# Kernel tuning notes

Hardware: AMD Instinct MI355X
Metric: run time of the kernel (lower is better)

## Reference

```python
import jax, jax.numpy as jnp
import numpy as np
import math

B, T = 2, 1024
D_MODEL = 1024
N_HEAD = 16
HEAD_DIM = D_MODEL // N_HEAD
VOCAB = 32000
NUM_LOOP = 4
EPS_LN = 1e-5                       # torch LayerNorm default
EPS_RMS = float(np.finfo(np.float32).eps)  # torch RMSNorm eps=None -> finfo eps


def setup_inputs() -> dict:
    key = jax.random.key(0)
    ks = jax.random.split(key, 12)
    s = 0.02
    d = D_MODEL
    tok = jax.random.normal(ks[1], (VOCAB, d), jnp.float32) * s
    tok = tok.at[0].set(0.0)  # padding_idx=0
    return {
        "idx": jax.random.randint(ks[0], (B, T), 0, VOCAB),
        "tok_embed": tok,
        "ln_e_g": jnp.ones((d,), jnp.float32),
        "ln_e_b": jnp.zeros((d,), jnp.float32),
        "Wqkv": jax.random.normal(ks[2], (d, 3 * d), jnp.float32) * s,
        "bqkv": jnp.zeros((3 * d,), jnp.float32),
        "Wo": jax.random.normal(ks[3], (d, d), jnp.float32) * s,
        "bo": jnp.zeros((d,), jnp.float32),
        "W1": jax.random.normal(ks[4], (d, 4 * d), jnp.float32) * s,
        "b1": jnp.zeros((4 * d,), jnp.float32),
        "W2": jax.random.normal(ks[5], (4 * d, d), jnp.float32) * s,
        "b2": jnp.zeros((d,), jnp.float32),
        "n1_w": jnp.ones((d,), jnp.float32),
        "n2_w": jnp.ones((d,), jnp.float32),
        "lnf_g": jnp.ones((d,), jnp.float32),
        "lnf_b": jnp.zeros((d,), jnp.float32),
        "Wlm": jax.random.normal(ks[6], (d, VOCAB), jnp.float32) * s,
        "blm": jnp.zeros((VOCAB,), jnp.float32),
    }


def layernorm(x, g, b):
    m = jnp.mean(x, axis=-1, keepdims=True)
    v = jnp.mean(jnp.square(x - m), axis=-1, keepdims=True)
    return (x - m) * jax.lax.rsqrt(v + EPS_LN) * g + b


def rmsnorm(x, w):
    ms = jnp.mean(jnp.square(x), axis=-1, keepdims=True)
    return x * jax.lax.rsqrt(ms + EPS_RMS) * w


def gelu_tanh(x):
    c = math.sqrt(2.0 / math.pi)
    return 0.5 * x * (1.0 + jnp.tanh(c * (x + 0.044715 * x * x * x)))


def alibi_causal_bias(t):
    # rpe[q,k] = -(q-k) for q>k else 0, scaled per head by 2^(-8/H*(h+1)); causal -inf above diag
    pos = jnp.arange(t)
    rel = pos[:, None] - pos[None, :]                      # [T,T] = q - k
    slopes = 2.0 ** (-8.0 / N_HEAD * jnp.arange(1, N_HEAD + 1, dtype=jnp.float32))
    bias = -slopes[:, None, None] * rel.astype(jnp.float32)  # [H,T,T]
    return jnp.where(rel[None] >= 0, bias, -jnp.inf)       # causal mask fused


def reference(idx, tok_embed, ln_e_g, ln_e_b, Wqkv, bqkv, Wo, bo,
              W1, b1, W2, b2, n1_w, n2_w, lnf_g, lnf_b, Wlm, blm):
    b, t = idx.shape
    x = layernorm(tok_embed[idx], ln_e_g, ln_e_b)          # rpe=True: no sinusoidal PE
    bias = alibi_causal_bias(t)                            # [H,T,T]
    scale = 1.0 / math.sqrt(HEAD_DIM)

    for _ in range(NUM_LOOP):
        # attention sublayer
        h = rmsnorm(x, n1_w)
        qkv = h @ Wqkv + bqkv
        q, k, v = jnp.split(qkv, 3, axis=-1)
        q = q.reshape(b, t, N_HEAD, HEAD_DIM).transpose(0, 2, 1, 3)
        k = k.reshape(b, t, N_HEAD, HEAD_DIM).transpose(0, 2, 1, 3)
        v = v.reshape(b, t, N_HEAD, HEAD_DIM).transpose(0, 2, 1, 3)
        att = jnp.einsum('bhqd,bhkd->bhqk', q, k) * scale + bias[None]
        att = jax.nn.softmax(att, axis=-1)
        y = jnp.einsum('bhqk,bhkd->bhqd', att, v)
        y = y.transpose(0, 2, 1, 3).reshape(b, t, D_MODEL)
        x = x + (y @ Wo + bo)
        # mlp sublayer
        h = rmsnorm(x, n2_w)
        x = x + (gelu_tanh(h @ W1 + b1) @ W2 + b2)

    x = layernorm(x, lnf_g, lnf_b)
    return x @ Wlm + blm  # [B,T,VOCAB]
```

## Files before the change

### kernel.cpp

```cpp
#include <hip/hip_runtime.h>
#include <stdint.h>

#define DEVI __device__ __forceinline__

typedef __attribute__((ext_vector_type(8))) short short8;
typedef __attribute__((ext_vector_type(4))) float f32x4;
typedef unsigned short u16;
typedef unsigned int u32;

typedef const __attribute__((address_space(1))) void* gas_ptr;
typedef __attribute__((address_space(3))) void* las_ptr;

constexpr int BBATCH = 2;
constexpr int TT  = 1024;
constexpr int BT  = BBATCH * TT;
constexpr int DM  = 1024;
constexpr int NH  = 16;
constexpr int HD  = 64;
constexpr int DFF = 4096;
constexpr int NV  = 32000;
constexpr int NL  = 4;

DEVI u16 f2b(float f) {
  u32 u = __builtin_bit_cast(u32, f);
  u = (u + 0x7fffu + ((u >> 16) & 1u)) >> 16;
  return (u16)u;
}
DEVI float b2f(u16 h) { return __builtin_bit_cast(float, (u32)h << 16); }

DEVI void gld16(const void* g, void* l) {
  __builtin_amdgcn_global_load_lds((gas_ptr)g, (las_ptr)l, 16, 0, 0);
}

DEVI float wave_sum(float v) {
#pragma unroll
  for (int off = 32; off; off >>= 1) v += __shfl_xor(v, off);
  return v;
}
DEVI float block_sum(float v, float* sb) {
  v = wave_sum(v);
  int lane = threadIdx.x & 63, wid = threadIdx.x >> 6;
  __syncthreads();
  if (lane == 0) sb[wid] = v;
  __syncthreads();
  return sb[0] + sb[1] + sb[2] + sb[3];
}

DEVI float gelu_f(float x) {
  float u = 0.7978845608028654f * (x + 0.044715f * x * x * x);
  float e = __expf(2.0f * u);
  return x * (1.0f - 1.0f / (e + 1.0f));
}

__global__ __launch_bounds__(256) void wt_transpose_all(
    const float* __restrict__ Wqkv, const float* __restrict__ Wo,
    const float* __restrict__ W1, const float* __restrict__ W2,
    const float* __restrict__ Wlm,
    u16* __restrict__ WqkvT, u16* __restrict__ WoT, u16* __restrict__ W1T,
    u16* __restrict__ W2T, u16* __restrict__ WlmT) {
  __shared__ float t[32][33];
  int bid = blockIdx.x;
  const float* in; u16* out; int K, N, tt;
  if (bid < 3072)       { in = Wqkv; out = WqkvT; K = 1024; N = 3072;  tt = bid; }
  else if (bid < 4096)  { in = Wo;   out = WoT;   K = 1024; N = 1024;  tt = bid - 3072; }
  else if (bid < 8192)  { in = W1;   out = W1T;   K = 1024; N = 4096;  tt = bid - 4096; }
  else if (bid < 12288) { in = W2;   out = W2T;   K = 4096; N = 1024;  tt = bid - 8192; }
  else                  { in = Wlm;  out = WlmT;  K = 1024; N = 32000; tt = bid - 12288; }
  int nx = N >> 5;
  int n0 = (tt % nx) * 32, k0 = (tt / nx) * 32;
  int tx = threadIdx.x & 31, ty = threadIdx.x >> 5;
#pragma unroll
  for (int i = 0; i < 4; ++i)
    t[ty + 8 * i][tx] = in[(size_t)(k0 + ty + 8 * i) * N + n0 + tx];
  __syncthreads();
#pragma unroll
  for (int i = 0; i < 4; ++i)
    out[(size_t)(n0 + ty + 8 * i) * K + k0 + tx] = f2b(t[tx][ty + 8 * i]);
}

__global__ __launch_bounds__(256) void embed_ln_k(const int* __restrict__ idx,
                                                  const float* __restrict__ tok,
                                                  const float* __restrict__ g,
                                                  const float* __restrict__ b,
                                                  float* __restrict__ x) {
  __shared__ float sb[4];
  int row = blockIdx.x, tid = threadIdx.x;
  float4 v = ((const float4*)(tok + (size_t)idx[row] * DM))[tid];
  float s = block_sum(v.x + v.y + v.z + v.w, sb);
  float m = s * (1.0f / DM);
  float dx = v.x - m, dy = v.y - m, dz = v.z - m, dw = v.w - m;
  float q = block_sum(dx * dx + dy * dy + dz * dz + dw * dw, sb);
  float rs = rsqrtf(q * (1.0f / DM) + 1e-5f);
  float4 gg = ((const float4*)g)[tid];
  float4 bb = ((const float4*)b)[tid];
  float4 o = make_float4(dx * rs * gg.x + bb.x, dy * rs * gg.y + bb.y,
                         dz * rs * gg.z + bb.z, dw * rs * gg.w + bb.w);
  ((float4*)(x + (size_t)row * DM))[tid] = o;
}

__global__ __launch_bounds__(256) void final_ln_k(const float* __restrict__ x,
                                                  const float* __restrict__ g,
                                                  const float* __restrict__ b,
                                                  u16* __restrict__ xf) {
  __shared__ float sb[4];
  int row = blockIdx.x, tid = threadIdx.x;
  float4 v = ((const float4*)(x + (size_t)row * DM))[tid];
  float s = block_sum(v.x + v.y + v.z + v.w, sb);
  float m = s * (1.0f / DM);
  float dx = v.x - m, dy = v.y - m, dz = v.z - m, dw = v.w - m;
  float q = block_sum(dx * dx + dy * dy + dz * dz + dw * dw, sb);
  float rs = rsqrtf(q * (1.0f / DM) + 1e-5f);
  float4 gg = ((const float4*)g)[tid];
  float4 bb = ((const float4*)b)[tid];
  u32 lo = (u32)f2b(dx * rs * gg.x + bb.x) | ((u32)f2b(dy * rs * gg.y + bb.y) << 16);
  u32 hi = (u32)f2b(dz * rs * gg.z + bb.z) | ((u32)f2b(dw * rs * gg.w + bb.w) << 16);
  ((uint2*)(xf + (size_t)row * DM))[tid] = make_uint2(lo, hi);
}

__global__ __launch_bounds__(256) void rmsnorm_k(const float* __restrict__ x,
                                                 const float* __restrict__ w,
                                                 u16* __restrict__ h) {
  __shared__ float sb[4];
  int row = blockIdx.x, tid = threadIdx.x;
  float4 v = ((const float4*)(x + (size_t)row * DM))[tid];
  float q = block_sum(v.x * v.x + v.y * v.y + v.z * v.z + v.w * v.w, sb);
  float rs = rsqrtf(q * (1.0f / DM) + 1.1920928955078125e-7f);
  float4 ww = ((const float4*)w)[tid];
  u32 lo = (u32)f2b(v.x * rs * ww.x) | ((u32)f2b(v.y * rs * ww.y) << 16);
  u32 hi = (u32)f2b(v.z * rs * ww.z) | ((u32)f2b(v.w * rs * ww.w) << 16);
  ((uint2*)(h + (size_t)row * DM))[tid] = make_uint2(lo, hi);
}

__global__ __launch_bounds__(256) void attn_k(const u16* __restrict__ qkv,
                                              const u16* __restrict__ vT,
                                              u16* __restrict__ y) {
  __shared__ __align__(16) char sP[16384];
  __shared__ __align__(16) char sK[16384];
  __shared__ __align__(16) char sV[16384];
  const int tid = threadIdx.x, lane = tid & 63, wid = tid >> 6;
  const int bid = blockIdx.x;
  const int sl = (bid + (bid >> 8)) & 15;
  const int qt = (sl & 1) ? (sl >> 1) : (15 - (sl >> 1));
  const int bh = (bid >> 4) & 31, b = bh >> 4, h = bh & 15;
  const int nt = (qt >> 1) + 1;
  const float slope = exp2f(-0.5f * (float)(h + 1));

  const char* Qb = (const char*)(qkv + (size_t)b * TT * 3 * DM + h * HD);
  const char* Kb = (const char*)(qkv + (size_t)b * TT * 3 * DM + DM + h * HD);
  const char* Vb = (const char*)(vT + (size_t)bh * HD * TT);

#pragma unroll
  for (int ci = 0; ci < 2; ++ci) {
    int c = wid * 2 + ci;
    int r = c * 8 + (lane >> 3);
    int q = (lane & 7) ^ (r & 7);
    gld16(Qb + (size_t)(qt * 64 + r) * 6144 + q * 16, sP + c * 1024 + lane * 16);
  }

  auto stageKV = [&](int kt) {
    int kv0 = kt * 128;
#pragma unroll
    for (int ci = 0; ci < 4; ++ci) {
      int c = wid * 4 + ci;
      int r = c * 8 + (lane >> 3);
      int q = (lane & 7) ^ (r & 7);
      gld16(Kb + (size_t)(kv0 + r) * 6144 + q * 16, sK + c * 1024 + lane * 16);
    }
#pragma unroll
    for (int ci = 0; ci < 4; ++ci) {
      int c = wid * 4 + ci;
      int d = c * 4 + (lane >> 4);
      int q = (lane & 15) ^ (d & 15);
      gld16(Vb + (size_t)d * 2048 + (size_t)kv0 * 2 + q * 16, sV + c * 1024 + lane * 16);
    }
  };
  stageKV(0);
  asm volatile("s_waitcnt vmcnt(8)" ::: "memory");

  short8 qf[2];
#pragma unroll
  for (int ks = 0; ks < 2; ++ks) {
    int r = wid * 16 + (lane & 15);
    int q = ((ks << 2) + (lane >> 4)) ^ (r & 7);
    qf[ks] = *(const short8*)(sP + r * 128 + q * 16);
  }

  f32x4 Y[4] = {};
  float m_r[4], l_r[4];
#pragma unroll
  for (int r = 0; r < 4; ++r) { m_r[r] = -3e38f; l_r[r] = 0.0f; }

  for (int kt = 0; kt < nt; ++kt) {
    asm volatile("s_waitcnt vmcnt(0)" ::: "memory");
    __syncthreads();

    f32x4 s[8] = {};
    __builtin_amdgcn_s_setprio(1);
#pragma unroll
    for (int ks = 0; ks < 2; ++ks) {
      short8 kf[8];
#pragma unroll
      for (int j = 0; j < 8; ++j) {
        int r = j * 16 + (lane & 15);
        int q = ((ks << 2) + (lane >> 4)) ^ (r & 7);
        kf[j] = *(const short8*)(sK + r * 128 + q * 16);
      }
#pragma unroll
      for (int j = 0; j < 8; ++j)
        s[j] = __builtin_amdgcn_mfma_f32_16x16x32_bf16(qf[ks], kf[j], s[j], 0, 0, 0);
    }
    __builtin_amdgcn_s_setprio(0);

    const int kv0 = kt * 128;
    const int qbase = qt * 64 + wid * 16 + ((lane >> 4) << 2);
    float rowmax[4] = {-3e38f, -3e38f, -3e38f, -3e38f};
#pragma unroll
    for (int j = 0; j < 8; ++j) {
      int kcol = kv0 + j * 16 + (lane & 15);
#pragma unroll
      for (int r = 0; r < 4; ++r) {
        int qrow = qbase + r;
        float v = (kcol <= qrow) ? s[j][r] * 0.125f - slope * (float)(qrow - kcol) : -3e38f;
        s[j][r] = v;
        rowmax[r] = fmaxf(rowmax[r], v);
      }
    }
#pragma unroll
    for (int r = 0; r < 4; ++r) {
      rowmax[r] = fmaxf(rowmax[r], __shfl_xor(rowmax[r], 1));
      rowmax[r] = fmaxf(rowmax[r], __shfl_xor(rowmax[r], 2));
      rowmax[r] = fmaxf(rowmax[r], __shfl_xor(rowmax[r], 4));
      rowmax[r] = fmaxf(rowmax[r], __shfl_xor(rowmax[r], 8));
      float mn = fmaxf(m_r[r], rowmax[r]);
      float al = __expf(m_r[r] - mn);
      m_r[r] = mn;
      l_r[r] *= al;
#pragma unroll
      for (int j = 0; j < 4; ++j) Y[j][r] *= al;
    }
    float rs[4] = {0.0f, 0.0f, 0.0f, 0.0f};
#pragma unroll
    for (int j = 0; j < 8; ++j)
#pragma unroll
      for (int r = 0; r < 4; ++r) {
        float p = __expf(s[j][r] - m_r[r]);
        s[j][r] = p;
        rs[r] += p;
      }
#pragma unroll
    for (int r = 0; r < 4; ++r) {
      rs[r] += __shfl_xor(rs[r], 1);
      rs[r] += __shfl_xor(rs[r], 2);
      rs[r] += __shfl_xor(rs[r], 4);
      rs[r] += __shfl_xor(rs[r], 8);
      l_r[r] += rs[r];
    }
#pragma unroll
    for (int j = 0; j < 8; ++j)
#pragma unroll
      for (int r = 0; r < 4; ++r) {
        int rl = wid * 16 + ((lane >> 4) << 2) + r;
        int c = j * 16 + (lane & 15);
        int g = c >> 3;
        *(u16*)(sP + rl * 256 + ((g ^ (rl & 15)) << 4) + (c & 7) * 2) = f2b(s[j][r]);
      }

    __builtin_amdgcn_s_setprio(1);
#pragma unroll
    for (int ks = 0; ks < 4; ++ks) {
      short8 pf, vf[4];
      {
        int r = wid * 16 + (lane & 15);
        int q = ((ks << 2) + (lane >> 4)) ^ (r & 15);
        pf = *(const short8*)(sP + r * 256 + (q << 4));
      }
#pragma unroll
      for (int j = 0; j < 4; ++j) {
        int d = j * 16 + (lane & 15);
        int q = ((ks << 2) + (lane >> 4)) ^ (d & 15);
        vf[j] = *(const short8*)(sV + d * 256 + (q << 4));
      }
#pragma unroll
      for (int j = 0; j < 4; ++j)
        Y[j] = __builtin_amdgcn_mfma_f32_16x16x32_bf16(pf, vf[j], Y[j], 0, 0, 0);
    }
    __builtin_amdgcn_s_setprio(0);
    __syncthreads();
    if (kt + 1 < nt) stageKV(kt + 1);
  }

#pragma unroll
  for (int r = 0; r < 4; ++r) {
    float inv = 1.0f / l_r[r];
    int qrow = qt * 64 + wid * 16 + ((lane >> 4) << 2) + r;
    u16* yp = y + (size_t)(b * TT + qrow) * DM + h * HD;
#pragma unroll
    for (int j = 0; j < 4; ++j)
      yp[j * 16 + (lane & 15)] = f2b(Y[j][r] * inv);
  }
}

enum { EPI_BF16 = 0, EPI_GELU = 1, EPI_ADDF32 = 2, EPI_F32 = 3, EPI_ATOMIC = 4, EPI_QKV = 5 };

template <int BM, int BN, int WM, int WN, int EPI, int KS = 1>
__global__ __launch_bounds__(256, 2) void gemm_bt(
    const u16* __restrict__ A, int lda, const u16* __restrict__ Bt, int ldb,
    const float* __restrict__ bias, void* __restrict__ C, int ldc,
    float* __restrict__ resid, int K, u16* __restrict__ vTout) {
  constexpr int BK = 64;
  constexpr int NW = WM * WN;
  constexpr int FM = BM / WM / 16, FN = BN / WN / 16;
  constexpr int ABYTES = BM * BK * 2, BBYTES = BN * BK * 2;
  constexpr int ACH = ABYTES / 1024, BCH = BBYTES / 1024, NCH = ACH + BCH;
  extern __shared__ __align__(16) char smem[];

  const int tid = threadIdx.x, lane = tid & 63, wid = tid >> 6;
  const int brow = blockIdx.y * BM, bcol = blockIdx.x * BN;
  const long long kbase2 = (long long)blockIdx.z * (K / KS) * 2;

  const int nt = (K / KS) >> 6;
  const int widm = wid / WN, widn = wid % WN;
  const int rm0 = widm * (BM / WM), cn0 = widn * (BN / WN);

  f32x4 acc[FM][FN] = {};

  const int swq16 = (((lane & 7) ^ ((lane >> 3) & 7)) << 4);
  const int lrow8 = lane >> 3;

  auto stage = [&](int buf, int kt) {
    char* base = smem + buf * (ABYTES + BBYTES);
    const char* Ag = (const char*)A;
    const char* Bg = (const char*)Bt;
    long long kOff = kbase2 + (long long)kt * 128 + swq16;
#pragma unroll
    for (int ci = 0; ci < NCH / NW; ++ci) {
      int c = wid + ci * NW;
      if (c < ACH) {
        int r = c * 8 + lrow8;
        gld16(Ag + (long long)(brow + r) * (lda * 2) + kOff, base + c * 1024 + lane * 16);
      } else {
        int r = (c - ACH) * 8 + lrow8;
        gld16(Bg + (long long)(bcol + r) * (ldb * 2) + kOff,
              base + ABYTES + (c - ACH) * 1024 + lane * 16);
      }
    }
  };

  auto compute = [&](int buf) {
    char* baseA = smem + buf * (ABYTES + BBYTES);
    char* baseB = baseA + ABYTES;
#pragma unroll
    for (int ks = 0; ks < 2; ++ks) {
      short8 af[FM], bv[FN];
#pragma unroll
      for (int i = 0; i < FM; ++i) {
        int r = rm0 + i * 16 + (lane & 15);
        int cq = ((ks << 2) + (lane >> 4)) ^ (r & 7);
        af[i] = *(const short8*)(baseA + r * 128 + (cq << 4));
      }
#pragma unroll
      for (int j = 0; j < FN; ++j) {
        int r = cn0 + j * 16 + (lane & 15);
        int cq = ((ks << 2) + (lane >> 4)) ^ (r & 7);
        bv[j] = *(const short8*)(baseB + r * 128 + (cq << 4));
      }
#pragma unroll
      for (int i = 0; i < FM; ++i)
#pragma unroll
        for (int j = 0; j < FN; ++j)
          acc[i][j] = __builtin_amdgcn_mfma_f32_16x16x32_bf16(af[i], bv[j], acc[i][j], 0, 0, 0);
    }
  };

  stage(0, 0);
  __syncthreads();
  int cur = 0;
  for (int t = 0; t < nt; ++t) {
    if (t + 1 < nt) stage(cur ^ 1, t + 1);
    compute(cur);
    __syncthreads();
    cur ^= 1;
  }

  if constexpr (EPI == EPI_QKV) {
    if (bcol >= 2 * DM) {
      u16* st = (u16*)smem;
#pragma unroll
      for (int i = 0; i < FM; ++i)
#pragma unroll
        for (int j = 0; j < FN; ++j)
#pragma unroll
          for (int r = 0; r < 4; ++r) {
            int rl = rm0 + i * 16 + ((lane >> 4) << 2) + r;
            int cl = cn0 + j * 16 + (lane & 15);
            st[rl * 130 + cl] = f2b(acc[i][j][r] + bias[bcol + cl]);
          }
      __syncthreads();
      const int b = brow >> 10, t0b = brow & (TT - 1);
      const int h0 = (bcol - 2 * DM) >> 6;
      const int sub = tid & 15;
#pragma unroll
      for (int pass = 0; pass < 8; ++pass) {
        int d = pass * 16 + (tid >> 4);
        u32 pk[4];
#pragma unroll
        for (int k2 = 0; k2 < 4; ++k2) {
          u16 lo = st[(sub * 8 + 2 * k2) * 130 + d];
          u16 hi = st[(sub * 8 + 2 * k2 + 1) * 130 + d];
          pk[k2] = (u32)lo | ((u32)hi << 16);
        }
        int head = h0 + (d >> 6), dd = d & 63;
        *(uint4*)(vTout + ((size_t)((b * NH + head) * HD + dd)) * TT + t0b + sub * 8) =
            make_uint4(pk[0], pk[1], pk[2], pk[3]);
      }
      return;
    }
  }

  const int r0 = brow + rm0 + ((lane >> 4) << 2);
  const int c0 = bcol + cn0 + (lane & 15);
#pragma unroll
  for (int i = 0; i < FM; ++i) {
#pragma unroll
    for (int j = 0; j < FN; ++j) {
#pragma unroll
      for (int r = 0; r < 4; ++r) {
        int row = r0 + i * 16 + r;
        int col = c0 + j * 16;
        float v = acc[i][j][r];
        if constexpr (EPI == EPI_BF16 || EPI == EPI_QKV) {
          ((u16*)C)[(size_t)row * ldc + col] = f2b(v + bias[col]);
        } else if constexpr (EPI == EPI_GELU) {
          ((u16*)C)[(size_t)row * ldc + col] = f2b(gelu_f(v + bias[col]));
        } else if constexpr (EPI == EPI_ADDF32) {
          size_t o = (size_t)row * ldc + col;
          resid[o] += v + bias[col];
        } else if constexpr (EPI == EPI_ATOMIC) {
          size_t o = (size_t)row * ldc + col;
          atomicAdd(&resid[o], v + (blockIdx.z == 0 ? bias[col] : 0.0f));
        } else {
          ((float*)C)[(size_t)row * ldc + col] = v + bias[col];
        }
      }
    }
  }
}

template <int EPI>
__global__ __launch_bounds__(512, 2) void gemm8(
    const u16* __restrict__ A, int lda, const u16* __restrict__ Bt, int ldb,
    const float* __restrict__ bias, void* __restrict__ C, int ldc, int K, int nby) {
  __shared__ __align__(16) char smem[2][2][32768];
  const int tid = threadIdx.x, lane = tid & 63;
  const int wid = tid >> 6, wm = wid >> 2, wn = wid & 3;

  const int nb = gridDim.x;
  const int q8 = nb >> 3, r8 = nb & 7;
  const int xcd = blockIdx.x & 7, lin = blockIdx.x >> 3;
  const int idx = (xcd < r8 ? xcd * (q8 + 1) : r8 * (q8 + 1) + (xcd - r8) * q8) + lin;
  const int brow = (idx % nby) * 256, bcol = (idx / nby) * 256;

  const int nt = K >> 6, niter = nt >> 1;

  const int srow = tid >> 3, sq = tid & 7;
  auto stage = [&](int buf, int isB, int half, int kt) {
    const u16* G = isB ? Bt : A;
    const int ld = isB ? ldb : lda;
    const int base = isB ? bcol : brow;
    char* L = &smem[buf][isB][half * 16384];
#pragma unroll
    for (int l = 0; l < 2; ++l) {
      int rl = half * 128 + l * 64 + srow;
      gld16((const char*)G + (size_t)(base + rl) * (ld * 2) + kt * 128 + ((sq ^ (rl & 7)) << 4),
            L + l * 8192 + tid * 16);
    }
  };

  short8 bfr[4][2], afr[2][2];
  f32x4 acc[8][4] = {};

  stage(0, 0, 0, 0); stage(0, 0, 1, 0);
  stage(0, 1, 0, 0); stage(0, 1, 1, 0);
  stage(1, 1, 0, 1); stage(1, 1, 1, 1);
  asm volatile("s_waitcnt vmcnt(0)" ::: "memory");
  __builtin_amdgcn_s_barrier();

  for (int i = 0; i < niter; ++i) {
    const bool full = (i + 1 < niter);
    const int t2 = 2 * i + 2, t3 = 2 * i + 3;
#pragma unroll
    for (int h = 0; h < 2; ++h) {
#pragma unroll
      for (int qd = 0; qd < 4; ++qd) {
        if (qd == 0) {
#pragma unroll
          for (int j = 0; j < 4; ++j)
#pragma unroll
            for (int ks = 0; ks < 2; ++ks) {
              int r = wn * 64 + j * 16 + (lane & 15);
              int q = ((ks << 2) + (lane >> 4)) ^ (r & 7);
              bfr[j][ks] = *(const short8*)&smem[h][1][r * 128 + q * 16];
            }
        }
#pragma unroll
        for (int f = 0; f < 2; ++f)
#pragma unroll
          for (int ks = 0; ks < 2; ++ks) {
            int r = wm * 128 + (qd * 2 + f) * 16 + (lane & 15);
            int q = ((ks << 2) + (lane >> 4)) ^ (r & 7);
            afr[f][ks] = *(const short8*)&smem[h][0][r * 128 + q * 16];
          }
        if (h == 0) {
          if (qd == 0) stage(1, 0, 0, 2 * i + 1);
          else if (qd == 1) stage(1, 0, 1, 2 * i + 1);
          else if (qd == 2) { if (full) stage(0, 1, 0, t2); }
          else              { if (full) stage(0, 1, 1, t2); }
        } else {
          if (qd == 0)      { if (full) stage(0, 0, 0, t2); }
          else if (qd == 1) { if (full) stage(0, 0, 1, t2); }
          else if (qd == 2) { if (full) stage(1, 1, 0, t3); }
          else              { if (full) stage(1, 1, 1, t3); }
        }
        if (qd == 3) {
          if (full) asm volatile("s_waitcnt vmcnt(4)" ::: "memory");
          else if (h == 0) asm volatile("s_waitcnt vmcnt(0)" ::: "memory");
        }
        __builtin_amdgcn_s_barrier();
        asm volatile("s_waitcnt lgkmcnt(0)" ::: "memory");
        __builtin_amdgcn_s_setprio(1);
#pragma unroll
        for (int f = 0; f < 2; ++f)
#pragma unroll
          for (int j = 0; j < 4; ++j)
#pragma unroll
            for (int ks = 0; ks < 2; ++ks)
              acc[qd * 2 + f][j] = __builtin_amdgcn_mfma_f32_16x16x32_bf16(
                  afr[f][ks], bfr[j][ks], acc[qd * 2 + f][j], 0, 0, 0);
        __builtin_amdgcn_s_setprio(0);
        __builtin_amdgcn_s_barrier();
      }
    }
  }

  if constexpr (EPI == EPI_F32) {
    char* sf = &smem[0][0][0];
    float* C32 = (float*)C;
#pragma unroll
    for (int half = 0; half < 2; ++half) {
      if (wm == half) {
#pragma unroll
        for (int fi = 0; fi < 8; ++fi)
#pragma unroll
          for (int j = 0; j < 4; ++j) {
            int cl = wn * 64 + j * 16 + (lane & 15);
            float bv = bias[bcol + cl];
            int qsw = (cl >> 2);
#pragma unroll
            for (int r = 0; r < 4; ++r) {
              int row = fi * 16 + ((lane >> 4) << 2) + r;
              *(float*)(sf + row * 1024 + ((qsw ^ (row & 7)) << 4) + (cl & 3) * 4) =
                  acc[fi][j][r] + bv;
            }
          }
      }
      __syncthreads();
#pragma unroll
      for (int pass = 0; pass < 16; ++pass) {
        int row = pass * 8 + wid;
        float4 v4 = *(float4*)(sf + row * 1024 + ((lane ^ (row & 7)) << 4));
        *(float4*)(C32 + (size_t)(brow + half * 128 + row) * ldc + bcol + lane * 4) = v4;
      }
      __syncthreads();
    }
    return;
  }

  const int r0 = brow + wm * 128 + ((lane >> 4) << 2);
  const int c0 = bcol + wn * 64 + (lane & 15);
#pragma unroll
  for (int fi = 0; fi < 8; ++fi) {
#pragma unroll
    for (int j = 0; j < 4; ++j) {
      int col = c0 + j * 16;
      float bv = bias[col];
#pragma unroll
      for (int r = 0; r < 4; ++r) {
        int row = r0 + fi * 16 + r;
        float v = acc[fi][j][r] + bv;
        if constexpr (EPI == EPI_GELU)
          ((u16*)C)[(size_t)row * ldc + col] = f2b(gelu_f(v));
        else
          ((u16*)C)[(size_t)row * ldc + col] = f2b(v);
      }
    }
  }
}

extern "C" void kernel_launch(void* const* d_in, const int* in_sizes, int n_in,
                              void* d_out, int out_size, void* d_ws, size_t ws_size,
                              hipStream_t stream) {
  (void)in_sizes; (void)n_in; (void)out_size;
  const int*   idx    = (const int*)d_in[0];
  const float* tok    = (const float*)d_in[1];
  const float* ln_e_g = (const float*)d_in[2];
  const float* ln_e_b = (const float*)d_in[3];
  const float* Wqkv   = (const float*)d_in[4];
  const float* bqkv   = (const float*)d_in[5];
  const float* Wo     = (const float*)d_in[6];
  const float* bo     = (const float*)d_in[7];
  const float* W1     = (const float*)d_in[8];
  const float* b1     = (const float*)d_in[9];
  const float* W2     = (const float*)d_in[10];
  const float* b2     = (const float*)d_in[11];
  const float* n1_w   = (const float*)d_in[12];
  const float* n2_w   = (const float*)d_in[13];
  const float* lnf_g  = (const float*)d_in[14];
  const float* lnf_b  = (const float*)d_in[15];
  const float* Wlm    = (const float*)d_in[16];
  const float* blm    = (const float*)d_in[17];
  float* out = (float*)d_out;

  char* w = (char*)d_ws;
  auto alloc = [&](size_t bytes) { char* p = w; w += (bytes + 255) & ~(size_t)255; return p; };
  float* x   = (float*)alloc((size_t)BT * DM * 4);
  u16* h     = (u16*)alloc((size_t)BT * DM * 2);
  u16* qkv   = (u16*)alloc((size_t)BT * 3 * DM * 2);
  u16* vT    = (u16*)alloc((size_t)BBATCH * NH * HD * TT * 2);
  u16* y     = (u16*)alloc((size_t)BT * DM * 2);
  u16* act   = (u16*)alloc((size_t)BT * DFF * 2);
  u16* xf    = (u16*)alloc((size_t)BT * DM * 2);
  u16* WqkvT = (u16*)alloc((size_t)3 * DM * DM * 2);
  u16* WoT   = (u16*)alloc((size_t)DM * DM * 2);
  u16* W1T   = (u16*)alloc((size_t)DFF * DM * 2);
  u16* W2T   = (u16*)alloc((size_t)DM * DFF * 2);
  u16* WlmT  = (u16*)alloc((size_t)NV * DM * 2);
  if ((size_t)(w - (char*)d_ws) > ws_size) return;

  wt_transpose_all<<<44288, 256, 0, stream>>>(Wqkv, Wo, W1, W2, Wlm,
                                              WqkvT, WoT, W1T, W2T, WlmT);

  embed_ln_k<<<BT, 256, 0, stream>>>(idx, tok, ln_e_g, ln_e_b, x);

  constexpr int SM128 = 2 * (128 * 64 * 2 + 128 * 64 * 2);
  constexpr int SM64  = 2 * (128 * 64 * 2 + 64 * 64 * 2);

  for (int l = 0; l < NL; ++l) {
    rmsnorm_k<<<BT, 256, 0, stream>>>(x, n1_w, h);
    gemm_bt<128, 128, 2, 2, EPI_QKV><<<dim3(3 * DM / 128, BT / 128), 256, SM128, stream>>>(
        h, DM, WqkvT, DM, bqkv, qkv, 3 * DM, nullptr, DM, vT);
    attn_k<<<512, 256, 0, stream>>>(qkv, vT, y);
    gemm_bt<128, 64, 4, 1, EPI_ATOMIC, 2><<<dim3(DM / 64, BT / 128, 2), 256, SM64, stream>>>(
        y, DM, WoT, DM, bo, nullptr, DM, x, DM, nullptr);
    rmsnorm_k<<<BT, 256, 0, stream>>>(x, n2_w, h);
    gemm_bt<128, 128, 2, 2, EPI_GELU><<<dim3(DFF / 128, BT / 128), 256, SM128, stream>>>(
        h, DM, W1T, DM, b1, act, DFF, nullptr, DM, nullptr);
    gemm_bt<128, 128, 2, 2, EPI_ATOMIC, 4><<<dim3(DM / 128, BT / 128, 4), 256, SM128, stream>>>(
        act, DFF, W2T, DFF, b2, nullptr, DM, x, DFF, nullptr);
  }

  final_ln_k<<<BT, 256, 0, stream>>>(x, lnf_g, lnf_b, xf);
  gemm8<EPI_F32><<<dim3((NV / 256) * (BT / 256)), 512, 0, stream>>>(
      xf, DM, WlmT, DM, blm, out, NV, DM, BT / 256);
}
```

Baseline: 851.5 us.

## Peel last GEMM k-iteration and interleave epilogue stores with final MMAs

The main loop now runs niter-1 iterations with no per-iteration tail checks. The final k-iteration is peeled, so its second half computes each quarter and immediately writes the bias-added results, overlapping stores with the remaining MFMAs. The LDS-staged, coalesced float32 epilogue is removed and replaced with direct scattered per-element float stores. That can hurt the large float32 LM-head output, which is the biggest GEMM here.

```diff
diff --git a/kernel.cpp b/kernel.cpp
--- a/kernel.cpp
+++ b/kernel.cpp
@@ -479,118 +479,114 @@
   short8 bfr[4][2], afr[2][2];
   f32x4 acc[8][4] = {};
 
+  auto LDB = [&](int h) {
+#pragma unroll
+    for (int j = 0; j < 4; ++j)
+#pragma unroll
+      for (int ks = 0; ks < 2; ++ks) {
+        int r = wn * 64 + j * 16 + (lane & 15);
+        int q = ((ks << 2) + (lane >> 4)) ^ (r & 7);
+        bfr[j][ks] = *(const short8*)&smem[h][1][r * 128 + q * 16];
+      }
+  };
+  auto LDA = [&](int h, int qd) {
+#pragma unroll
+    for (int f = 0; f < 2; ++f)
+#pragma unroll
+      for (int ks = 0; ks < 2; ++ks) {
+        int r = wm * 128 + (qd * 2 + f) * 16 + (lane & 15);
+        int q = ((ks << 2) + (lane >> 4)) ^ (r & 7);
+        afr[f][ks] = *(const short8*)&smem[h][0][r * 128 + q * 16];
+      }
+  };
+  auto MMA = [&](int qd) {
+#pragma unroll
+    for (int f = 0; f < 2; ++f)
+#pragma unroll
+      for (int j = 0; j < 4; ++j)
+#pragma unroll
+        for (int ks = 0; ks < 2; ++ks)
+          acc[qd * 2 + f][j] = __builtin_amdgcn_mfma_f32_16x16x32_bf16(
+              afr[f][ks], bfr[j][ks], acc[qd * 2 + f][j], 0, 0, 0);
+  };
+
   stage(0, 0, 0, 0); stage(0, 0, 1, 0);
   stage(0, 1, 0, 0); stage(0, 1, 1, 0);
   stage(1, 1, 0, 1); stage(1, 1, 1, 1);
   asm volatile("s_waitcnt vmcnt(0)" ::: "memory");
   __builtin_amdgcn_s_barrier();
 
-  for (int i = 0; i < niter; ++i) {
-    const bool full = (i + 1 < niter);
+  for (int i = 0; i < niter - 1; ++i) {
     const int t2 = 2 * i + 2, t3 = 2 * i + 3;
 #pragma unroll
     for (int h = 0; h < 2; ++h) {
 #pragma unroll
       for (int qd = 0; qd < 4; ++qd) {
-        if (qd == 0) {
-#pragma unroll
-          for (int j = 0; j < 4; ++j)
-#pragma unroll
-            for (int ks = 0; ks < 2; ++ks) {
-              int r = wn * 64 + j * 16 + (lane & 15);
-              int q = ((ks << 2) + (lane >> 4)) ^ (r & 7);
-              bfr[j][ks] = *(const short8*)&smem[h][1][r * 128 + q * 16];
-            }
-        }
-#pragma unroll
-        for (int f = 0; f < 2; ++f)
-#pragma unroll
-          for (int ks = 0; ks < 2; ++ks) {
-            int r = wm * 128 + (qd * 2 + f) * 16 + (lane & 15);
-            int q = ((ks << 2) + (lane >> 4)) ^ (r & 7);
-            afr[f][ks] = *(const short8*)&smem[h][0][r * 128 + q * 16];
-          }
+        if (qd == 0) LDB(h);
+        LDA(h, qd);
         if (h == 0) {
           if (qd == 0) stage(1, 0, 0, 2 * i + 1);
           else if (qd == 1) stage(1, 0, 1, 2 * i + 1);
-          else if (qd == 2) { if (full) stage(0, 1, 0, t2); }
-          else              { if (full) stage(0, 1, 1, t2); }
+          else if (qd == 2) stage(0, 1, 0, t2);
+          else              stage(0, 1, 1, t2);
         } else {
-          if (qd == 0)      { if (full) stage(0, 0, 0, t2); }
-          else if (qd == 1) { if (full) stage(0, 0, 1, t2); }
-          else if (qd == 2) { if (full) stage(1, 1, 0, t3); }
-          else              { if (full) stage(1, 1, 1, t3); }
+          if (qd == 0)      stage(0, 0, 0, t2);
+          else if (qd == 1) stage(0, 0, 1, t2);
+          else if (qd == 2) stage(1, 1, 0, t3);
+          else              stage(1, 1, 1, t3);
         }
-        if (qd == 3) {
-          if (full) asm volatile("s_waitcnt vmcnt(4)" ::: "memory");
-          else if (h == 0) asm volatile("s_waitcnt vmcnt(0)" ::: "memory");
-        }
+        if (qd == 3) asm volatile("s_waitcnt vmcnt(4)" ::: "memory");
         __builtin_amdgcn_s_barrier();
         asm volatile("s_waitcnt lgkmcnt(0)" ::: "memory");
         __builtin_amdgcn_s_setprio(1);
-#pragma unroll
-        for (int f = 0; f < 2; ++f)
-#pragma unroll
-          for (int j = 0; j < 4; ++j)
-#pragma unroll
-            for (int ks = 0; ks < 2; ++ks)
-              acc[qd * 2 + f][j] = __builtin_amdgcn_mfma_f32_16x16x32_bf16(
-                  afr[f][ks], bfr[j][ks], acc[qd * 2 + f][j], 0, 0, 0);
+        MMA(qd);
         __builtin_amdgcn_s_setprio(0);
         __builtin_amdgcn_s_barrier();
       }
     }
   }
 
-  if constexpr (EPI == EPI_F32) {
-    char* sf = &smem[0][0][0];
-    float* C32 = (float*)C;
-#pragma unroll
-    for (int half = 0; half < 2; ++half) {
-      if (wm == half) {
-#pragma unroll
-        for (int fi = 0; fi < 8; ++fi)
-#pragma unroll
-          for (int j = 0; j < 4; ++j) {
-            int cl = wn * 64 + j * 16 + (lane & 15);
-            float bv = bias[bcol + cl];
-            int qsw = (cl >> 2);
-#pragma unroll
-            for (int r = 0; r < 4; ++r) {
-              int row = fi * 16 + ((lane >> 4) << 2) + r;
-              *(float*)(sf + row * 1024 + ((qsw ^ (row & 7)) << 4) + (cl & 3) * 4) =
-                  acc[fi][j][r] + bv;
-            }
-          }
-      }
-      __syncthreads();
-#pragma unroll
-      for (int pass = 0; pass < 16; ++pass) {
-        int row = pass * 8 + wid;
-        float4 v4 = *(float4*)(sf + row * 1024 + ((lane ^ (row & 7)) << 4));
-        *(float4*)(C32 + (size_t)(brow + half * 128 + row) * ldc + bcol + lane * 4) = v4;
-      }
-      __syncthreads();
-    }
-    return;
-  }
-
+#pragma unroll
+  for (int qd = 0; qd < 4; ++qd) {
+    if (qd == 0) LDB(0);
+    LDA(0, qd);
+    if (qd == 0) stage(1, 0, 0, nt - 1);
+    else if (qd == 1) stage(1, 0, 1, nt - 1);
+    if (qd == 3) asm volatile("s_waitcnt vmcnt(0)" ::: "memory");
+    __builtin_amdgcn_s_barrier();
+    asm volatile("s_waitcnt lgkmcnt(0)" ::: "memory");
+    __builtin_amdgcn_s_setprio(1);
+    MMA(qd);
+    __builtin_amdgcn_s_setprio(0);
+    __builtin_amdgcn_s_barrier();
+  }
   const int r0 = brow + wm * 128 + ((lane >> 4) << 2);
   const int c0 = bcol + wn * 64 + (lane & 15);
 #pragma unroll
-  for (int fi = 0; fi < 8; ++fi) {
-#pragma unroll
-    for (int j = 0; j < 4; ++j) {
-      int col = c0 + j * 16;
-      float bv = bias[col];
-#pragma unroll
-      for (int r = 0; r < 4; ++r) {
-        int row = r0 + fi * 16 + r;
-        float v = acc[fi][j][r] + bv;
-        if constexpr (EPI == EPI_GELU)
-          ((u16*)C)[(size_t)row * ldc + col] = f2b(gelu_f(v));
-        else
-          ((u16*)C)[(size_t)row * ldc + col] = f2b(v);
+  for (int qd = 0; qd < 4; ++qd) {
+    if (qd == 0) LDB(1);
+    LDA(1, qd);
+    __builtin_amdgcn_s_setprio(1);
+    MMA(qd);
+    __builtin_amdgcn_s_setprio(0);
+#pragma unroll
+    for (int f = 0; f < 2; ++f) {
+      int fi = qd * 2 + f;
+#pragma unroll
+      for (int j = 0; j < 4; ++j) {
+        int col = c0 + j * 16;
+        float bv = bias[col];
+#pragma unroll
+        for (int r = 0; r < 4; ++r) {
+          int row = r0 + fi * 16 + r;
+          float v = acc[fi][j][r] + bv;
+          if constexpr (EPI == EPI_F32)
+            ((float*)C)[(size_t)row * ldc + col] = v;
+          else if constexpr (EPI == EPI_GELU)
+            ((u16*)C)[(size_t)row * ldc + col] = f2b(gelu_f(v));
+          else
+            ((u16*)C)[(size_t)row * ldc + col] = f2b(v);
+        }
       }
     }
   }
```

Result: no change. 847.9 us (-0.4%).
